# Kernel tuning notes

Hardware: AMD Instinct MI355X
Metric: run time of the kernel (lower is better)

The kernel has to match this reference:

```python
import jax, jax.numpy as jnp
import numpy as np

N_INP = 512
N_HID = 512
BATCH = 64
STEPS = 512


def setup_inputs() -> dict:
    key = jax.random.key(0)
    ks = jax.random.split(key, 7)

    def xavier(k, n_in, n_out):
        bound = np.sqrt(3.0) * np.sqrt(2.0 / float(n_in + n_out))
        return jax.random.uniform(k, (n_in, n_out), jnp.float32, -bound, bound)

    return {
        "inputs": jax.random.normal(ks[0], (BATCH, STEPS, N_INP), jnp.float32),
        "W_xz": xavier(ks[1], N_INP, N_HID),
        "W_hz": xavier(ks[2], N_HID, N_HID),
        "b_z": jnp.zeros((N_HID,), jnp.float32),
        "W_xr": xavier(ks[3], N_INP, N_HID),
        "W_hr": xavier(ks[4], N_HID, N_HID),
        "b_r": jnp.zeros((N_HID,), jnp.float32),
        "W_xh": xavier(ks[5], N_INP, N_HID),
        "W_hh": xavier(ks[6], N_HID, N_HID),
        "b_h": jnp.zeros((N_HID,), jnp.float32),
        "train": 0,
    }


def reference(inputs, W_xz, W_hz, b_z, W_xr, W_hr, b_r, W_xh, W_hh, b_h, train):
    # inputs: (B, T, n_inp). GRU with eval-mode (dropout_rate=0), so the
    # dropout branch in the original forward is a no-op.
    B = inputs.shape[0]
    H0 = jnp.zeros((B, W_hz.shape[0]), inputs.dtype)

    def step(H_t, X_t):
        Z_t = jax.nn.sigmoid(X_t @ W_xz + H_t @ W_hz + b_z)
        R_t = jax.nn.sigmoid(X_t @ W_xr + H_t @ W_hr + b_r)
        H_tilde = jnp.tanh(X_t @ W_xh + (R_t * H_t) @ W_hh + b_h)
        H_new = Z_t * H_t + (1.0 - Z_t) * H_tilde
        return H_new, H_new

    xs = jnp.swapaxes(inputs, 0, 1)  # (T, B, n_inp)
    H_final, outs = jax.lax.scan(step, H0, xs)
    outputs = jnp.swapaxes(outs, 0, 1)  # (B, T, n_hid)
    return outputs, H_final
```

## Files before the change

### kernel.cpp

```cpp
#include <hip/hip_runtime.h>

#define B_   64
#define T_   512
#define KIN  512
#define NH   512
#define KEFF 3072
#define NBLK 64
#define NTHR 512

typedef __attribute__((ext_vector_type(8))) short short8;
typedef __attribute__((ext_vector_type(4))) float f32x4;
typedef __attribute__((ext_vector_type(4))) unsigned int u32x4;

__device__ __forceinline__ unsigned short f2b(float f) {
    union { float f; unsigned int u; } v; v.f = f;
    unsigned int u = v.u;
    return (unsigned short)((u + 0x7FFFu + ((u >> 16) & 1u)) >> 16);
}
__device__ __forceinline__ float b2f(unsigned short h) {
    union { float f; unsigned int u; } v; v.u = ((unsigned int)h) << 16;
    return v.f;
}

__global__ void prepack(const float* __restrict__ Wxz, const float* __restrict__ Whz,
                        const float* __restrict__ Wxr, const float* __restrict__ Whr,
                        const float* __restrict__ Wxh, const float* __restrict__ Whh,
                        unsigned short* __restrict__ Bzr, unsigned short* __restrict__ Bh) {
    int keff = blockIdx.x * 256 + threadIdx.x;
    int n    = blockIdx.y;
    int seg  = keff >> 9;
    int k    = keff & 511;
    const float* src;
    int c;
    if (n < 512)       { c = n;        src = (seg < 3) ? Whz : Wxz; }
    else if (n < 1024) { c = n - 512;  src = (seg < 3) ? Whr : Wxr; }
    else               { c = n - 1024; src = (seg < 3) ? Whh : Wxh; }
    float w = src[k * NH + c];
    unsigned short hi = f2b(w);
    unsigned short o  = (seg == 2 || seg == 5) ? f2b(w - b2f(hi)) : hi;
    if (n < 1024) Bzr[(size_t)n * KEFF + keff] = o;
    else          Bh[(size_t)(n - 1024) * KEFF + keff] = o;
}

__device__ __forceinline__ unsigned int ald32(const unsigned int* p) {
    return __hip_atomic_load(p, __ATOMIC_RELAXED, __HIP_MEMORY_SCOPE_AGENT);
}
__device__ __forceinline__ unsigned long long ald64(const void* p) {
    return __hip_atomic_load((const unsigned long long*)p, __ATOMIC_RELAXED,
                             __HIP_MEMORY_SCOPE_AGENT);
}
__device__ __forceinline__ void ast32(unsigned int* p, unsigned int v) {
    __hip_atomic_store(p, v, __ATOMIC_RELAXED, __HIP_MEMORY_SCOPE_AGENT);
}
__device__ __forceinline__ void ast64(void* p, unsigned long long v) {
    __hip_atomic_store((unsigned long long*)p, v, __ATOMIC_RELAXED,
                       __HIP_MEMORY_SCOPE_AGENT);
}

__device__ __forceinline__ void flag_wait(const unsigned int* flags,
                                          unsigned int tgt, int lane) {
    while (1) {
        unsigned int v = ald32(flags + lane);
        if (__all((int)(v >= tgt))) break;
    }
    __builtin_amdgcn_sched_barrier(0);
}

__device__ __forceinline__ int hp_idx(int m, int c) {
    return m * 512 + (c ^ ((m & 7) << 2));
}

__device__ __forceinline__ void cvt_x8(const float* xr, int kp, short8* ahi, short8* alo) {
    f32x4 x0 = *(const f32x4*)(xr + kp);
    f32x4 x1 = *(const f32x4*)(xr + kp + 4);
#pragma unroll
    for (int i = 0; i < 4; ++i) {
        unsigned short h0 = f2b(x0[i]);
        (*ahi)[i] = (short)h0; (*alo)[i] = (short)f2b(x0[i] - b2f(h0));
        unsigned short h1 = f2b(x1[i]);
        (*ahi)[4 + i] = (short)h1; (*alo)[4 + i] = (short)f2b(x1[i] - b2f(h1));
    }
}

__device__ __forceinline__ void unpackw(u32x4 w0, u32x4 w1, short8* ahi, short8* alo) {
    union { unsigned int u[4]; short8 v; } H, L;
    H.u[0] = __builtin_amdgcn_perm(w0[1], w0[0], 0x05040100u);
    H.u[1] = __builtin_amdgcn_perm(w0[3], w0[2], 0x05040100u);
    H.u[2] = __builtin_amdgcn_perm(w1[1], w1[0], 0x05040100u);
    H.u[3] = __builtin_amdgcn_perm(w1[3], w1[2], 0x05040100u);
    L.u[0] = __builtin_amdgcn_perm(w0[1], w0[0], 0x07060302u);
    L.u[1] = __builtin_amdgcn_perm(w0[3], w0[2], 0x07060302u);
    L.u[2] = __builtin_amdgcn_perm(w1[1], w1[0], 0x07060302u);
    L.u[3] = __builtin_amdgcn_perm(w1[3], w1[2], 0x07060302u);
    *ahi = H.v; *alo = L.v;
}

#define MFMA(a, b, c) __builtin_amdgcn_mfma_f32_16x16x32_bf16((a), (b), (c), 0, 0, 0)

__global__ void __launch_bounds__(NTHR, 2) gru_seq(
    const float* __restrict__ X, const float* __restrict__ bz,
    const float* __restrict__ br, const float* __restrict__ bh,
    float* __restrict__ out, float* __restrict__ Zt,
    unsigned int* __restrict__ HP, unsigned int* __restrict__ RHP,
    const unsigned short* __restrict__ Bzr, const unsigned short* __restrict__ Bh,
    unsigned int* flags) {
    const int blk  = blockIdx.x;
    const int tid  = threadIdx.x;
    const int wv   = tid >> 6;
    const int hwv  = wv & 3;
    const bool xcrew = wv >= 4;
    const int lane = tid & 63;
    const int fm   = lane & 15;
    const int fkc  = lane >> 4;
    const int fk   = fkc * 8;

    __shared__ unsigned int hbuf[4 * 16 * 512];
    __shared__ float xp1[2][4][16][16];
    __shared__ float xp2a[2][2][16][16];
    __shared__ float xp2b[2][2][16][16];
    __shared__ float comb[2][256];

    const int m1 = hwv * 16 + fm;
    const unsigned short* Bp1 = Bzr + (size_t)(blk * 16 + fm) * KEFF;
    const int c1 = blk * 16 + fm;

    const int mt  = blk & 3;
    const int s2i = hwv >> 1;
    const int jh  = hwv & 1;
    const int nt  = (blk >> 2) * 2 + s2i;
    const int m2  = mt * 16 + fm;
    const unsigned short* Bp2 = Bh + (size_t)(nt * 16 + fm) * KEFF;
    const int c2 = nt * 16 + fm;

    const int key = (fm & 7) << 4;
    const int sw0 = (32 * fkc) ^ key;
    const int sw1 = (32 * fkc + 16) ^ key;
    const char* HPb  = (const char*)HP;
    const char* RHPb = (const char*)RHP;

    const float bias1 = (blk < 32) ? bz[c1] : br[c1 - 512];
    const float bhi   = bh[c2];

    auto xg1 = [&](int tt, int buf) {
        f32x4 acc = {0.f, 0.f, 0.f, 0.f};
        const float* xr = X + (size_t)m1 * (T_ * KIN) + (size_t)tt * KIN;
#pragma unroll 4
        for (int j = 0; j < 16; ++j) {
            int kp = j * 32 + fk;
            short8 xhi, xlo; cvt_x8(xr, kp, &xhi, &xlo);
            short8 b3 = *(const short8*)(Bp1 + 1536 + kp);
            short8 b4 = *(const short8*)(Bp1 + 2048 + kp);
            short8 b5 = *(const short8*)(Bp1 + 2560 + kp);
            acc = MFMA(xhi, b3, acc); acc = MFMA(xlo, b4, acc); acc = MFMA(xhi, b5, acc);
        }
#pragma unroll
        for (int jj = 0; jj < 4; ++jj) xp1[buf][hwv][fkc * 4 + jj][fm] = acc[jj];
    };
    auto xg2 = [&](int tt, int buf) {
        f32x4 acc = {0.f, 0.f, 0.f, 0.f};
        const float* xr = X + (size_t)m2 * (T_ * KIN) + (size_t)tt * KIN;
#pragma unroll
        for (int j = jh * 8; j < jh * 8 + 8; ++j) {
            int kp = j * 32 + fk;
            short8 xhi, xlo; cvt_x8(xr, kp, &xhi, &xlo);
            short8 b3 = *(const short8*)(Bp2 + 1536 + kp);
            short8 b4 = *(const short8*)(Bp2 + 2048 + kp);
            short8 b5 = *(const short8*)(Bp2 + 2560 + kp);
            acc = MFMA(xhi, b3, acc); acc = MFMA(xlo, b4, acc); acc = MFMA(xhi, b5, acc);
        }
        float (*dst)[16][16] = jh ? xp2b[buf] : xp2a[buf];
#pragma unroll
        for (int jj = 0; jj < 4; ++jj) dst[s2i][fkc * 4 + jj][fm] = acc[jj];
    };

    if (xcrew) { xg1(0, 0); xg2(0, 0); }
    __syncthreads();

    for (int t = 0; t < T_; ++t) {
        const int bufc = t & 1, bufn = bufc ^ 1;
        const unsigned int ep = (unsigned int)t * 2u;
        if (wv == 0 && t) flag_wait(flags, ep, lane);
        __syncthreads();
        if (!xcrew) {
            const char* src = HPb + hwv * 32768;
            char* dst = (char*)hbuf + hwv * 32768;
#pragma unroll
            for (int i = 0; i < 32; ++i)
                __builtin_amdgcn_global_load_lds(
                    (const unsigned int*)(src + i * 1024 + lane * 16),
                    (unsigned int*)(dst + i * 1024), 16, 0, 0x11);
            asm volatile("s_waitcnt vmcnt(0)" ::: "memory");
            __builtin_amdgcn_sched_barrier(0);
            f32x4 acc = {0.f, 0.f, 0.f, 0.f};
            const char* sl = (const char*)hbuf + hwv * 32768 + fm * 2048;
#pragma unroll 4
            for (int j = 0; j < 16; ++j) {
                u32x4 w0 = *(const u32x4*)(sl + 128 * j + sw0);
                u32x4 w1 = *(const u32x4*)(sl + 128 * j + sw1);
                short8 ahi, alo; unpackw(w0, w1, &ahi, &alo);
                int kp = j * 32 + fk;
                short8 b0 = *(const short8*)(Bp1 + kp);
                short8 b1 = *(const short8*)(Bp1 + 512 + kp);
                short8 b2 = *(const short8*)(Bp1 + 1024 + kp);
                acc = MFMA(ahi, b0, acc); acc = MFMA(alo, b1, acc); acc = MFMA(ahi, b2, acc);
            }
            if (blk < 32) {
                float g[4];
#pragma unroll
                for (int jj = 0; jj < 4; ++jj)
                    g[jj] = 1.f / (1.f + __expf(-(acc[jj] +
                              xp1[bufc][hwv][fkc * 4 + jj][fm] + bias1)));
                union { float f[2]; unsigned long long q; } p0, p1;
                p0.f[0] = g[0]; p0.f[1] = g[1];
                p1.f[0] = g[2]; p1.f[1] = g[3];
                float* zp = Zt + c1 * 64 + hwv * 16 + fkc * 4;
                ast64(zp, p0.q); ast64(zp + 2, p1.q);
            } else {
                int cr = c1 - 512;
#pragma unroll
                for (int jj = 0; jj < 4; ++jj) {
                    int lr = fkc * 4 + jj;
                    unsigned int hw = *(const unsigned int*)((const char*)hbuf +
                        hwv * 32768 + lr * 2048 + ((4 * cr) ^ ((lr & 7) << 4)));
                    float h  = b2f((unsigned short)(hw & 0xffffu)) +
                               b2f((unsigned short)(hw >> 16));
                    float gr = 1.f / (1.f + __expf(-(acc[jj] +
                                 xp1[bufc][hwv][lr][fm] + bias1)));
                    float rh = gr * h;
                    unsigned short hi = f2b(rh);
                    unsigned short lo = f2b(rh - b2f(hi));
                    ast32(RHP + hp_idx(hwv * 16 + lr, cr),
                          (unsigned int)hi | ((unsigned int)lo << 16));
                }
            }
        } else if (t + 1 < T_) {
            xg1(t + 1, bufn);
        }
        __syncthreads();
        if (tid == 0) ast32(flags + blk, ep + 1u);
        if (wv == 0) flag_wait(flags, ep + 1u, lane);
        if (xcrew && t + 1 < T_) xg2(t + 1, bufn);
        __syncthreads();
        unsigned long long zq0 = 0, zq1 = 0;
        if (!xcrew) {
            if (jh == 0) {
                const float* zp = Zt + c2 * 64 + mt * 16 + fkc * 4;
                zq0 = ald64(zp); zq1 = ald64(zp + 2);
            }
            const char* srcR = RHPb + mt * 32768;
            char* dstR = (char*)hbuf + ((mt + 2) & 3) * 32768;
#pragma unroll
            for (int i = 0; i < 8; ++i) {
                int o = (hwv * 8 + i) * 1024;
                __builtin_amdgcn_global_load_lds(
                    (const unsigned int*)(srcR + o + lane * 16),
                    (unsigned int*)(dstR + o), 16, 0, 0x11);
            }
            asm volatile("s_waitcnt vmcnt(0)" ::: "memory");
            __builtin_amdgcn_sched_barrier(0);
        }
        __syncthreads();
        f32x4 acc2 = {0.f, 0.f, 0.f, 0.f};
        if (!xcrew) {
            const char* sl2 = (const char*)hbuf + ((mt + 2) & 3) * 32768 + fm * 2048;
#pragma unroll
            for (int j = jh * 8; j < jh * 8 + 8; ++j) {
                u32x4 w0 = *(const u32x4*)(sl2 + 128 * j + sw0);
                u32x4 w1 = *(const u32x4*)(sl2 + 128 * j + sw1);
                short8 ahi, alo; unpackw(w0, w1, &ahi, &alo);
                int kp = j * 32 + fk;
                short8 b0 = *(const short8*)(Bp2 + kp);
                short8 b1 = *(const short8*)(Bp2 + 512 + kp);
                short8 b2 = *(const short8*)(Bp2 + 1024 + kp);
                acc2 = MFMA(ahi, b0, acc2); acc2 = MFMA(alo, b1, acc2); acc2 = MFMA(ahi, b2, acc2);
            }
            if (jh == 1) {
#pragma unroll
                for (int jj = 0; jj < 4; ++jj)
                    comb[s2i][(fkc * 4 + jj) * 16 + fm] = acc2[jj];
            }
        }
        __syncthreads();
        if (!xcrew && jh == 0) {
            union { unsigned long long q; float f[2]; } z0, z1;
            z0.q = zq0; z1.q = zq1;
            float zv[4] = {z0.f[0], z0.f[1], z1.f[0], z1.f[1]};
#pragma unroll
            for (int jj = 0; jj < 4; ++jj) {
                int lr   = fkc * 4 + jj;
                int mrow = mt * 16 + lr;
                unsigned int hw = *(const unsigned int*)((const char*)hbuf +
                    mt * 32768 + lr * 2048 + ((4 * c2) ^ ((lr & 7) << 4)));
                float h   = b2f((unsigned short)(hw & 0xffffu)) +
                            b2f((unsigned short)(hw >> 16));
                float pre = acc2[jj] + comb[s2i][lr * 16 + fm] +
                            xp2a[bufc][s2i][lr][fm] + xp2b[bufc][s2i][lr][fm] + bhi;
                float e   = __expf(-2.f * pre);
                float ht  = 2.f / (1.f + e) - 1.f;
                float hn  = zv[jj] * h + (1.f - zv[jj]) * ht;
                out[(size_t)mrow * (T_ * NH) + (size_t)t * NH + c2] = hn;
                if (t == T_ - 1)
                    out[(size_t)B_ * T_ * NH + mrow * NH + c2] = hn;
                unsigned short hi = f2b(hn);
                unsigned short lo = f2b(hn - b2f(hi));
                ast32(HP + hp_idx(mrow, c2),
                      (unsigned int)hi | ((unsigned int)lo << 16));
            }
        }
        __syncthreads();
        if (tid == 0) ast32(flags + blk, ep + 2u);
    }
}

extern "C" void kernel_launch(void* const* d_in, const int* in_sizes, int n_in,
                              void* d_out, int out_size, void* d_ws, size_t ws_size,
                              hipStream_t stream) {
    (void)in_sizes; (void)n_in; (void)out_size; (void)ws_size;
    const float* X   = (const float*)d_in[0];
    const float* Wxz = (const float*)d_in[1];
    const float* Whz = (const float*)d_in[2];
    const float* bz  = (const float*)d_in[3];
    const float* Wxr = (const float*)d_in[4];
    const float* Whr = (const float*)d_in[5];
    const float* br  = (const float*)d_in[6];
    const float* Wxh = (const float*)d_in[7];
    const float* Whh = (const float*)d_in[8];
    const float* bh  = (const float*)d_in[9];
    float* out = (float*)d_out;

    char* ws = (char*)d_ws;
    unsigned int* flags = (unsigned int*)ws;
    float* Zt         = (float*)(ws + 256);
    unsigned int* HP  = (unsigned int*)(ws + 256 + 131072);
    unsigned int* RHP = (unsigned int*)(ws + 256 + 262144);
    unsigned short* Bzr = (unsigned short*)(ws + (1 << 20));
    unsigned short* Bh  = Bzr + (size_t)1024 * KEFF;

    hipMemsetAsync(d_ws, 0, 1 << 20, stream);
    prepack<<<dim3(12, 1536), 256, 0, stream>>>(Wxz, Whz, Wxr, Whr, Wxh, Whh, Bzr, Bh);
    gru_seq<<<NBLK, NTHR, 0, stream>>>(X, bz, br, bh, out, Zt, HP, RHP, Bzr, Bh, flags);
}
```

Before: 14.47 ms.

## Partition GRU blocks into independent batch groups with per-group barriers

Blocks are reorganized into four batch groups of 16 rows, each handled by 16 blocks that own slices of the hidden columns and synchronize only among themselves through per-group flags. Each block now stages only its group's 16-row hidden state and reset-scaled state into shared memory, instead of all 64 rows. This shrinks the per-step global-to-LDS traffic and narrows each grid barrier to 16 participants. In exchange every block streams the full weight rows for more columns, and an extra block-wide sync is added after the hidden-state load.

```diff
diff --git a/kernel.cpp b/kernel.cpp
--- a/kernel.cpp
+++ b/kernel.cpp
@@ -57,10 +57,10 @@
                        __HIP_MEMORY_SCOPE_AGENT);
 }
 
-__device__ __forceinline__ void flag_wait(const unsigned int* flags,
-                                          unsigned int tgt, int lane) {
+__device__ __forceinline__ void flag_wait16(const unsigned int* flg,
+                                            unsigned int tgt, int fidx) {
     while (1) {
-        unsigned int v = ald32(flags + lane);
+        unsigned int v = ald32(flg + fidx);
         if (__all((int)(v >= tgt))) break;
     }
     __builtin_amdgcn_sched_barrier(0);
@@ -104,46 +104,50 @@
     unsigned int* __restrict__ HP, unsigned int* __restrict__ RHP,
     const unsigned short* __restrict__ Bzr, const unsigned short* __restrict__ Bh,
     unsigned int* flags) {
-    const int blk  = blockIdx.x;
+    const int bid  = blockIdx.x;
+    const int s    = bid & 15;
+    const int g    = bid >> 4;
     const int tid  = threadIdx.x;
     const int wv   = tid >> 6;
-    const int hwv  = wv & 3;
-    const bool xcrew = wv >= 4;
+    const int w4   = wv & 3;
+    const bool xc  = wv >= 4;
     const int lane = tid & 63;
     const int fm   = lane & 15;
     const int fkc  = lane >> 4;
     const int fk   = fkc * 8;
 
-    __shared__ unsigned int hbuf[4 * 16 * 512];
+    __shared__ unsigned int hbufH[16 * 512];
+    __shared__ unsigned int hbufR[16 * 512];
     __shared__ float xp1[2][4][16][16];
     __shared__ float xp2a[2][2][16][16];
     __shared__ float xp2b[2][2][16][16];
     __shared__ float comb[2][256];
 
-    const int m1 = hwv * 16 + fm;
-    const unsigned short* Bp1 = Bzr + (size_t)(blk * 16 + fm) * KEFF;
-    const int c1 = blk * 16 + fm;
-
-    const int mt  = blk & 3;
-    const int s2i = hwv >> 1;
-    const int jh  = hwv & 1;
-    const int nt  = (blk >> 2) * 2 + s2i;
-    const int m2  = mt * 16 + fm;
-    const unsigned short* Bp2 = Bh + (size_t)(nt * 16 + fm) * KEFF;
-    const int c2 = nt * 16 + fm;
+    const int c1 = s * 64 + w4 * 16 + fm;
+    const unsigned short* Bp1 = Bzr + (size_t)c1 * KEFF;
+    const bool isz = (c1 < 512);
+    const float bias1 = isz ? bz[c1] : br[c1 - 512];
+
+    const int ti = w4 >> 1, jh = w4 & 1;
+    const int c2 = s * 32 + ti * 16 + fm;
+    const unsigned short* Bp2 = Bh + (size_t)c2 * KEFF;
+    const float bias2 = bh[c2];
 
     const int key = (fm & 7) << 4;
     const int sw0 = (32 * fkc) ^ key;
     const int sw1 = (32 * fkc + 16) ^ key;
-    const char* HPb  = (const char*)HP;
-    const char* RHPb = (const char*)RHP;
-
-    const float bias1 = (blk < 32) ? bz[c1] : br[c1 - 512];
-    const float bhi   = bh[c2];
+
+    unsigned int* HPg  = HP  + g * 8192;
+    unsigned int* RHPg = RHP + g * 8192;
+    float*        Ztg  = Zt  + g * 8192;
+    unsigned int* flg  = flags + g * 32;
+    const int fidx = (lane < 16) ? lane : 15;
+
+    const float* Xg = X + (size_t)(16 * g + fm) * (T_ * KIN);
 
     auto xg1 = [&](int tt, int buf) {
         f32x4 acc = {0.f, 0.f, 0.f, 0.f};
-        const float* xr = X + (size_t)m1 * (T_ * KIN) + (size_t)tt * KIN;
+        const float* xr = Xg + (size_t)tt * KIN;
 #pragma unroll 4
         for (int j = 0; j < 16; ++j) {
             int kp = j * 32 + fk;
@@ -154,11 +158,11 @@
             acc = MFMA(xhi, b3, acc); acc = MFMA(xlo, b4, acc); acc = MFMA(xhi, b5, acc);
         }
 #pragma unroll
-        for (int jj = 0; jj < 4; ++jj) xp1[buf][hwv][fkc * 4 + jj][fm] = acc[jj];
+        for (int jj = 0; jj < 4; ++jj) xp1[buf][w4][fkc * 4 + jj][fm] = acc[jj];
     };
     auto xg2 = [&](int tt, int buf) {
         f32x4 acc = {0.f, 0.f, 0.f, 0.f};
-        const float* xr = X + (size_t)m2 * (T_ * KIN) + (size_t)tt * KIN;
+        const float* xr = Xg + (size_t)tt * KIN;
 #pragma unroll
         for (int j = jh * 8; j < jh * 8 + 8; ++j) {
             int kp = j * 32 + fk;
@@ -170,29 +174,34 @@
         }
         float (*dst)[16][16] = jh ? xp2b[buf] : xp2a[buf];
 #pragma unroll
-        for (int jj = 0; jj < 4; ++jj) dst[s2i][fkc * 4 + jj][fm] = acc[jj];
+        for (int jj = 0; jj < 4; ++jj) dst[ti][fkc * 4 + jj][fm] = acc[jj];
     };
 
-    if (xcrew) { xg1(0, 0); xg2(0, 0); }
+    if (xc) { xg1(0, 0); xg2(0, 0); }
     __syncthreads();
 
     for (int t = 0; t < T_; ++t) {
         const int bufc = t & 1, bufn = bufc ^ 1;
         const unsigned int ep = (unsigned int)t * 2u;
-        if (wv == 0 && t) flag_wait(flags, ep, lane);
-        __syncthreads();
-        if (!xcrew) {
-            const char* src = HPb + hwv * 32768;
-            char* dst = (char*)hbuf + hwv * 32768;
-#pragma unroll
-            for (int i = 0; i < 32; ++i)
+        if (wv == 0 && t) flag_wait16(flg, ep, fidx);
+        __syncthreads();
+        if (!xc) {
+            const char* srcb = (const char*)HPg;
+            char* dstb = (char*)hbufH;
+#pragma unroll
+            for (int i = 0; i < 8; ++i) {
+                int r = w4 * 8 + i;
                 __builtin_amdgcn_global_load_lds(
-                    (const unsigned int*)(src + i * 1024 + lane * 16),
-                    (unsigned int*)(dst + i * 1024), 16, 0, 0x11);
+                    (const unsigned int*)(srcb + r * 1024 + lane * 16),
+                    (unsigned int*)(dstb + r * 1024), 16, 0, 0x11);
+            }
             asm volatile("s_waitcnt vmcnt(0)" ::: "memory");
             __builtin_amdgcn_sched_barrier(0);
+        }
+        __syncthreads();
+        if (!xc) {
             f32x4 acc = {0.f, 0.f, 0.f, 0.f};
-            const char* sl = (const char*)hbuf + hwv * 32768 + fm * 2048;
+            const char* sl = (const char*)hbufH + fm * 2048;
 #pragma unroll 4
             for (int j = 0; j < 16; ++j) {
                 u32x4 w0 = *(const u32x4*)(sl + 128 * j + sw0);
@@ -204,32 +213,32 @@
                 short8 b2 = *(const short8*)(Bp1 + 1024 + kp);
                 acc = MFMA(ahi, b0, acc); acc = MFMA(alo, b1, acc); acc = MFMA(ahi, b2, acc);
             }
-            if (blk < 32) {
-                float g[4];
+            if (isz) {
+                float gz[4];
 #pragma unroll
                 for (int jj = 0; jj < 4; ++jj)
-                    g[jj] = 1.f / (1.f + __expf(-(acc[jj] +
-                              xp1[bufc][hwv][fkc * 4 + jj][fm] + bias1)));
+                    gz[jj] = 1.f / (1.f + __expf(-(acc[jj] +
+                               xp1[bufc][w4][fkc * 4 + jj][fm] + bias1)));
                 union { float f[2]; unsigned long long q; } p0, p1;
-                p0.f[0] = g[0]; p0.f[1] = g[1];
-                p1.f[0] = g[2]; p1.f[1] = g[3];
-                float* zp = Zt + c1 * 64 + hwv * 16 + fkc * 4;
+                p0.f[0] = gz[0]; p0.f[1] = gz[1];
+                p1.f[0] = gz[2]; p1.f[1] = gz[3];
+                float* zp = Ztg + c1 * 16 + fkc * 4;
                 ast64(zp, p0.q); ast64(zp + 2, p1.q);
             } else {
                 int cr = c1 - 512;
 #pragma unroll
                 for (int jj = 0; jj < 4; ++jj) {
-                    int lr = fkc * 4 + jj;
-                    unsigned int hw = *(const unsigned int*)((const char*)hbuf +
-                        hwv * 32768 + lr * 2048 + ((4 * cr) ^ ((lr & 7) << 4)));
+                    int mr = fkc * 4 + jj;
+                    unsigned int hw = *(const unsigned int*)((const char*)hbufH +
+                        mr * 2048 + ((4 * cr) ^ ((mr & 7) << 4)));
                     float h  = b2f((unsigned short)(hw & 0xffffu)) +
                                b2f((unsigned short)(hw >> 16));
                     float gr = 1.f / (1.f + __expf(-(acc[jj] +
-                                 xp1[bufc][hwv][lr][fm] + bias1)));
+                                 xp1[bufc][w4][mr][fm] + bias1)));
                     float rh = gr * h;
                     unsigned short hi = f2b(rh);
                     unsigned short lo = f2b(rh - b2f(hi));
-                    ast32(RHP + hp_idx(hwv * 16 + lr, cr),
+                    ast32(RHPg + hp_idx(mr, cr),
                           (unsigned int)hi | ((unsigned int)lo << 16));
                 }
             }
@@ -237,32 +246,32 @@
             xg1(t + 1, bufn);
         }
         __syncthreads();
-        if (tid == 0) ast32(flags + blk, ep + 1u);
-        if (wv == 0) flag_wait(flags, ep + 1u, lane);
-        if (xcrew && t + 1 < T_) xg2(t + 1, bufn);
+        if (tid == 0) ast32(flg + s, ep + 1u);
+        if (wv == 0) flag_wait16(flg, ep + 1u, fidx);
+        else if (xc && t + 1 < T_) xg2(t + 1, bufn);
         __syncthreads();
         unsigned long long zq0 = 0, zq1 = 0;
-        if (!xcrew) {
+        if (!xc) {
             if (jh == 0) {
-                const float* zp = Zt + c2 * 64 + mt * 16 + fkc * 4;
+                const float* zp = Ztg + c2 * 16 + fkc * 4;
                 zq0 = ald64(zp); zq1 = ald64(zp + 2);
             }
-            const char* srcR = RHPb + mt * 32768;
-            char* dstR = (char*)hbuf + ((mt + 2) & 3) * 32768;
+            const char* srcb = (const char*)RHPg;
+            char* dstb = (char*)hbufR;
 #pragma unroll
             for (int i = 0; i < 8; ++i) {
-                int o = (hwv * 8 + i) * 1024;
+                int r = w4 * 8 + i;
                 __builtin_amdgcn_global_load_lds(
-                    (const unsigned int*)(srcR + o + lane * 16),
-                    (unsigned int*)(dstR + o), 16, 0, 0x11);
+                    (const unsigned int*)(srcb + r * 1024 + lane * 16),
+                    (unsigned int*)(dstb + r * 1024), 16, 0, 0x11);
             }
             asm volatile("s_waitcnt vmcnt(0)" ::: "memory");
             __builtin_amdgcn_sched_barrier(0);
         }
         __syncthreads();
         f32x4 acc2 = {0.f, 0.f, 0.f, 0.f};
-        if (!xcrew) {
-            const char* sl2 = (const char*)hbuf + ((mt + 2) & 3) * 32768 + fm * 2048;
+        if (!xc) {
+            const char* sl2 = (const char*)hbufR + fm * 2048;
 #pragma unroll
             for (int j = jh * 8; j < jh * 8 + 8; ++j) {
                 u32x4 w0 = *(const u32x4*)(sl2 + 128 * j + sw0);
@@ -277,38 +286,38 @@
             if (jh == 1) {
 #pragma unroll
                 for (int jj = 0; jj < 4; ++jj)
-                    comb[s2i][(fkc * 4 + jj) * 16 + fm] = acc2[jj];
-            }
-        }
-        __syncthreads();
-        if (!xcrew && jh == 0) {
+                    comb[ti][(fkc * 4 + jj) * 16 + fm] = acc2[jj];
+            }
+        }
+        __syncthreads();
+        if (!xc && jh == 0) {
             union { unsigned long long q; float f[2]; } z0, z1;
             z0.q = zq0; z1.q = zq1;
             float zv[4] = {z0.f[0], z0.f[1], z1.f[0], z1.f[1]};
 #pragma unroll
             for (int jj = 0; jj < 4; ++jj) {
-                int lr   = fkc * 4 + jj;
-                int mrow = mt * 16 + lr;
-                unsigned int hw = *(const unsigned int*)((const char*)hbuf +
-                    mt * 32768 + lr * 2048 + ((4 * c2) ^ ((lr & 7) << 4)));
+                int mr = fkc * 4 + jj;
+                unsigned int hw = *(const unsigned int*)((const char*)hbufH +
+                    mr * 2048 + ((4 * c2) ^ ((mr & 7) << 4)));
                 float h   = b2f((unsigned short)(hw & 0xffffu)) +
                             b2f((unsigned short)(hw >> 16));
-                float pre = acc2[jj] + comb[s2i][lr * 16 + fm] +
-                            xp2a[bufc][s2i][lr][fm] + xp2b[bufc][s2i][lr][fm] + bhi;
+                float pre = acc2[jj] + comb[ti][mr * 16 + fm] +
+                            xp2a[bufc][ti][mr][fm] + xp2b[bufc][ti][mr][fm] + bias2;
                 float e   = __expf(-2.f * pre);
                 float ht  = 2.f / (1.f + e) - 1.f;
                 float hn  = zv[jj] * h + (1.f - zv[jj]) * ht;
-                out[(size_t)mrow * (T_ * NH) + (size_t)t * NH + c2] = hn;
+                int mg = 16 * g + mr;
+                out[(size_t)mg * (T_ * NH) + (size_t)t * NH + c2] = hn;
                 if (t == T_ - 1)
-                    out[(size_t)B_ * T_ * NH + mrow * NH + c2] = hn;
+                    out[(size_t)B_ * T_ * NH + mg * NH + c2] = hn;
                 unsigned short hi = f2b(hn);
                 unsigned short lo = f2b(hn - b2f(hi));
-                ast32(HP + hp_idx(mrow, c2),
+                ast32(HPg + hp_idx(mr, c2),
                       (unsigned int)hi | ((unsigned int)lo << 16));
             }
         }
         __syncthreads();
-        if (tid == 0) ast32(flags + blk, ep + 2u);
+        if (tid == 0) ast32(flg + s, ep + 2u);
     }
 }
 
@@ -330,9 +339,9 @@
 
     char* ws = (char*)d_ws;
     unsigned int* flags = (unsigned int*)ws;
-    float* Zt         = (float*)(ws + 256);
-    unsigned int* HP  = (unsigned int*)(ws + 256 + 131072);
-    unsigned int* RHP = (unsigned int*)(ws + 256 + 262144);
+    float* Zt         = (float*)(ws + 8192);
+    unsigned int* HP  = (unsigned int*)(ws + 8192 + 131072);
+    unsigned int* RHP = (unsigned int*)(ws + 8192 + 262144);
     unsigned short* Bzr = (unsigned short*)(ws + (1 << 20));
     unsigned short* Bh  = Bzr + (size_t)1024 * KEFF;
 
```

After: 13.24 ms. 1.09x faster.
